# Kernel tuning notes

Measured on AMD Instinct MI355X. Metric: run time of the kernel, lower is better.

Reference implementation:

```python
import jax, jax.numpy as jnp
import numpy as np

B, S, D = 4, 2048, 1024
E, H, TOP_K = 8, 4096, 2


def setup_inputs() -> dict:
    key = jax.random.key(0)
    ks = jax.random.split(key, 5)
    scale = 0.02
    return {
        "x": jax.random.normal(ks[0], (B, S, D), dtype=jnp.float32),
        "Wr": jax.random.normal(ks[1], (D, E), dtype=jnp.float32) * scale,
        "br": jnp.zeros((E,), dtype=jnp.float32),
        "W1": jax.random.normal(ks[2], (E, D, H), dtype=jnp.float32) * scale,
        "b1": jnp.zeros((E, H), dtype=jnp.float32),
        "W2": jax.random.normal(ks[3], (E, H, D), dtype=jnp.float32) * scale,
        "b2": jnp.zeros((E, D), dtype=jnp.float32),
    }


def reference(x, Wr, br, W1, b1, W2, b2):
    b, s, d = x.shape
    xf = x.reshape(-1, d)                                   # [T, D]
    gate = jax.nn.softmax(xf @ Wr + br, axis=-1)            # [T, E]
    top_w, top_i = jax.lax.top_k(gate, TOP_K)               # [T, K]
    top_w = top_w / jnp.sum(top_w, axis=-1, keepdims=True)
    # combine[t, e] = sum_i top_w[t, i] * 1{top_i[t, i] == e}
    combine = jnp.sum(jax.nn.one_hot(top_i, E, dtype=xf.dtype) * top_w[..., None], axis=1)  # [T, E]
    # Dense all-expert FFN (same math as the masked per-expert loops in torch)
    h = jax.nn.gelu(jnp.einsum('td,edh->teh', xf, W1) + b1, approximate=False)  # [T, E, H]
    out = jnp.einsum('teh,ehd,te->td', h, W2, combine) + combine @ b2           # [T, D]
    return out.reshape(b, s, d)
```

## Files before the change

### kernel.cpp

```cpp
#include <hip/hip_runtime.h>
#include <cstdio>


#define T_TOK 8192
#define DIM   1024
#define NEXP  8
#define HID   4096
#define MAXR  18432

typedef float          f32x4   __attribute__((ext_vector_type(4)));
typedef short          bf16x8  __attribute__((ext_vector_type(8)));
typedef unsigned short u16x4   __attribute__((ext_vector_type(4)));

static __device__ __forceinline__ unsigned short f2bf(float f) {
  unsigned int u = __builtin_bit_cast(unsigned int, f);
  u = (u + 0x7FFFu + ((u >> 16) & 1u)) >> 16;
  return (unsigned short)u;
}

static __device__ __forceinline__ void gl16(const void* g, void* l) {
  __builtin_amdgcn_global_load_lds(
      (const __attribute__((address_space(1))) unsigned int*)g,
      (__attribute__((address_space(3))) unsigned int*)l,
      16, 0, 0);
}

#define FENCE() asm volatile("" ::: "memory")

__global__ __launch_bounds__(256) void router_k(const float* __restrict__ x,
                                                const float* __restrict__ Wr,
                                                const float* __restrict__ br,
                                                int* __restrict__ meta,
                                                int2* __restrict__ top_i,
                                                float2* __restrict__ top_w) {
  int lane = threadIdx.x & 63;
  int wid  = threadIdx.x >> 6;
  int t = blockIdx.x * 4 + wid;
  const float* xp = x + (size_t)t * DIM + lane * 16;
  float acc[NEXP];
#pragma unroll
  for (int e = 0; e < NEXP; ++e) acc[e] = 0.f;
#pragma unroll
  for (int j = 0; j < 16; j += 4) {
    float4 xv = *(const float4*)(xp + j);
    const float* wp = Wr + (size_t)(lane * 16 + j) * NEXP;
#pragma unroll
    for (int jj = 0; jj < 4; ++jj) {
      float xs = jj == 0 ? xv.x : jj == 1 ? xv.y : jj == 2 ? xv.z : xv.w;
      float4 w0 = *(const float4*)(wp + jj * NEXP);
      float4 w1 = *(const float4*)(wp + jj * NEXP + 4);
      acc[0] += xs * w0.x; acc[1] += xs * w0.y; acc[2] += xs * w0.z; acc[3] += xs * w0.w;
      acc[4] += xs * w1.x; acc[5] += xs * w1.y; acc[6] += xs * w1.z; acc[7] += xs * w1.w;
    }
  }
#pragma unroll
  for (int off = 32; off > 0; off >>= 1) {
#pragma unroll
    for (int e = 0; e < NEXP; ++e) acc[e] += __shfl_xor(acc[e], off);
  }
  if (lane == 0) {
    float l[NEXP];
#pragma unroll
    for (int e = 0; e < NEXP; ++e) l[e] = acc[e] + br[e];
    int e1 = 0;
#pragma unroll
    for (int e = 1; e < NEXP; ++e) if (l[e] > l[e1]) e1 = e;
    int e2 = (e1 == 0) ? 1 : 0;
#pragma unroll
    for (int e = 0; e < NEXP; ++e) if (e != e1 && l[e] > l[e2]) e2 = e;
    float g  = expf(l[e2] - l[e1]);
    float w1 = 1.f / (1.f + g);
    top_i[t] = make_int2(e1, e2);
    top_w[t] = make_float2(w1, 1.f - w1);
    atomicAdd(&meta[e1], 1);
    atomicAdd(&meta[e2], 1);
  }
}

__global__ void prefix_k(int* __restrict__ meta) {
  if (threadIdx.x == 0) {
    int s = 0;
#pragma unroll
    for (int e = 0; e < NEXP; ++e) {
      meta[16 + e] = s;
      s += (meta[e] + 255) & ~255;
    }
    meta[24] = s;
    meta[25] = s;
  }
}

__global__ __launch_bounds__(256) void fill_k(int* __restrict__ tok_of_row,
                                              float* __restrict__ wt_of_row) {
  int i = blockIdx.x * 256 + threadIdx.x;
  if (i < MAXR) { tok_of_row[i] = 0; wt_of_row[i] = 0.f; }
}

__global__ __launch_bounds__(256) void scatter_k(const int2* __restrict__ top_i,
                                                 const float2* __restrict__ top_w,
                                                 int* __restrict__ meta,
                                                 int* __restrict__ row_of,
                                                 int* __restrict__ tok_of_row,
                                                 float* __restrict__ wt_of_row) {
  int t = blockIdx.x * 256 + threadIdx.x;
  int2  ei = top_i[t];
  float2 w = top_w[t];
  int p = atomicAdd(&meta[8 + ei.x], 1);
  int r = meta[16 + ei.x] + p;
  tok_of_row[r] = t; wt_of_row[r] = w.x; row_of[t * 2] = r;
  p = atomicAdd(&meta[8 + ei.y], 1);
  r = meta[16 + ei.y] + p;
  tok_of_row[r] = t; wt_of_row[r] = w.y; row_of[t * 2 + 1] = r;
}

__global__ __launch_bounds__(256) void gather_k(const float* __restrict__ x,
                                                const int* __restrict__ tok_of_row,
                                                const int* __restrict__ meta,
                                                unsigned short* __restrict__ xg) {
  int r = blockIdx.x;
  if (r >= meta[25]) return;
  int t = tok_of_row[r];
  int c = threadIdx.x * 4;
  float4 v = *(const float4*)(x + (size_t)t * DIM + c);
  u16x4 o;
  o[0] = f2bf(v.x); o[1] = f2bf(v.y); o[2] = f2bf(v.z); o[3] = f2bf(v.w);
  *(u16x4*)(xg + (size_t)r * DIM + c) = o;
}

__global__ __launch_bounds__(256) void transpose_convert_k(const float* __restrict__ W,
                                                           unsigned short* __restrict__ WT,
                                                           int R, int C) {
  __shared__ float tile[32][33];
  int e = blockIdx.z;
  int c0 = blockIdx.x * 32, r0 = blockIdx.y * 32;
  const float* Wp = W + (size_t)e * R * C;
  unsigned short* Op = WT + (size_t)e * R * C;
  int tr = threadIdx.x >> 3;
  int tc = (threadIdx.x & 7) * 4;
  float4 v = *(const float4*)(Wp + (size_t)(r0 + tr) * C + c0 + tc);
  tile[tr][tc] = v.x; tile[tr][tc + 1] = v.y; tile[tr][tc + 2] = v.z; tile[tr][tc + 3] = v.w;
  __syncthreads();
  int oc  = threadIdx.x >> 3;
  int orr = (threadIdx.x & 7) * 4;
  u16x4 o;
#pragma unroll
  for (int j = 0; j < 4; ++j) o[j] = f2bf(tile[orr + j][oc]);
  *(u16x4*)(Op + (size_t)(c0 + oc) * R + r0 + orr) = o;
}


template <int KH, int MH>
__device__ __forceinline__ void do_phase(const unsigned short* lds_, int buf,
                                         int aoff, int boff, f32x4 (&acc)[8][4]) {
  const unsigned short* Ar = lds_ + (buf * 4 + KH) * 8192 + aoff + MH * 2048;
  const unsigned short* Br = lds_ + (buf * 4 + 2 + KH) * 8192 + boff;
  bf16x8 af[4], bv[4];
#pragma unroll
  for (int r = 0; r < 4; ++r) af[r] = *(const bf16x8*)(Ar + r * 512);
#pragma unroll
  for (int n = 0; n < 4; ++n) bv[n] = *(const bf16x8*)(Br + n * 512);
  __builtin_amdgcn_s_setprio(1);
#pragma unroll
  for (int r = 0; r < 4; ++r)
#pragma unroll
    for (int n = 0; n < 4; ++n)
      acc[MH * 4 + r][n] =
          __builtin_amdgcn_mfma_f32_16x16x32_bf16(af[r], bv[n], acc[MH * 4 + r][n], 0, 0, 0);
  __builtin_amdgcn_s_setprio(0);
}

template <int KTOT, int NTOT, int EPI>
__global__ __launch_bounds__(512, 2) void gemm8_k(const unsigned short* __restrict__ A,
                                                  const unsigned short* __restrict__ Bt,
                                                  const float* __restrict__ bias,
                                                  const int* __restrict__ meta,
                                                  const float* __restrict__ wt_of_row,
                                                  const int* __restrict__ tok_of_row,
                                                  void* __restrict__ Cout) {
  constexpr int NTILES = NTOT / 256;
  constexpr int NWG = (MAXR / 256) * NTILES;
  constexpr int NT = KTOT / 64;
  __shared__ __align__(16) unsigned short lds[65536];

  int id = ((int)blockIdx.x & 7) * (NWG / 8) + ((int)blockIdx.x >> 3);
  int row0 = (id / NTILES) * 256;
  int n0   = (id % NTILES) * 256;
  if (row0 >= meta[25]) return;
  int e = 0;
  while (meta[17 + e] <= row0) ++e;
  const unsigned short* Bp = Bt + (size_t)e * NTOT * KTOT;

  int tid = threadIdx.x;
  int lane = tid & 63, wid = tid >> 6;
  int wm = wid >> 2, wn = wid & 3;

  int r0s = tid >> 2, r1s = 128 + (tid >> 2);
  int s0 = (tid & 3) ^ ((r0s >> 1) & 3);
  int s1 = (tid & 3) ^ ((r1s >> 1) & 3);
  const unsigned short* pA0 = A + (size_t)(row0 + r0s) * KTOT + s0 * 8;
  const unsigned short* pA1 = A + (size_t)(row0 + r1s) * KTOT + s1 * 8;
  const unsigned short* pB0 = Bp + (size_t)(n0 + r0s) * KTOT + s0 * 8;
  const unsigned short* pB1 = Bp + (size_t)(n0 + r1s) * KTOT + s1 * 8;
  int ldst = wid * 512;

  auto stage = [&](int bufx, int mat, int kh, int kt) {
    int rb = (bufx * 4 + mat * 2 + kh) * 8192 + ldst;
    int ko = kt * 64 + kh * 32;
    gl16((mat ? pB0 : pA0) + ko, (void*)(lds + rb));
    gl16((mat ? pB1 : pA1) + ko, (void*)(lds + rb + 4096));
  };

  int sF = ((lane >> 4) ^ ((lane >> 1) & 3)) * 8;
  int aoff = wm * 4096 + (lane & 15) * 32 + sF;
  int boff = wn * 2048 + (lane & 15) * 32 + sF;

  f32x4 acc[8][4];
#pragma unroll
  for (int r = 0; r < 8; ++r)
#pragma unroll
    for (int n = 0; n < 4; ++n) acc[r][n] = (f32x4){0.f, 0.f, 0.f, 0.f};

  stage(0, 1, 0, 0); stage(0, 0, 0, 0); stage(0, 1, 1, 0); stage(0, 0, 1, 0);
  FENCE();

  for (int t = 0; t < NT - 1; ++t) {
    int buf = t & 1, nb = buf ^ 1;
    stage(nb, 1, 0, t + 1);
    asm volatile("s_waitcnt vmcnt(6)" ::: "memory");
    __builtin_amdgcn_s_barrier(); FENCE();
    do_phase<0, 0>(lds, buf, aoff, boff, acc);
    stage(nb, 0, 0, t + 1); FENCE();
    __builtin_amdgcn_s_barrier(); FENCE();
    do_phase<0, 1>(lds, buf, aoff, boff, acc);
    stage(nb, 1, 1, t + 1);
    asm volatile("s_waitcnt vmcnt(6)" ::: "memory");
    __builtin_amdgcn_s_barrier(); FENCE();
    do_phase<1, 0>(lds, buf, aoff, boff, acc);
    stage(nb, 0, 1, t + 1); FENCE();
    __builtin_amdgcn_s_barrier(); FENCE();
    do_phase<1, 1>(lds, buf, aoff, boff, acc);
  }
  {
    int buf = (NT - 1) & 1;
    asm volatile("s_waitcnt vmcnt(4)" ::: "memory");
    __builtin_amdgcn_s_barrier(); FENCE();
    do_phase<0, 0>(lds, buf, aoff, boff, acc);
    __builtin_amdgcn_s_barrier(); FENCE();
    do_phase<0, 1>(lds, buf, aoff, boff, acc);
    asm volatile("s_waitcnt vmcnt(0)" ::: "memory");
    __builtin_amdgcn_s_barrier(); FENCE();
    do_phase<1, 0>(lds, buf, aoff, boff, acc);
    __builtin_amdgcn_s_barrier(); FENCE();
    do_phase<1, 1>(lds, buf, aoff, boff, acc);
  }

  int rb2 = row0 + wm * 128 + ((lane >> 4) << 2);
  int nb2 = n0 + wn * 64 + (lane & 15);
  if constexpr (EPI == 0) {
    unsigned short* Hp = (unsigned short*)Cout;
    const float* bp = bias + (size_t)e * NTOT;
#pragma unroll
    for (int r = 0; r < 8; ++r)
#pragma unroll
      for (int n = 0; n < 4; ++n) {
        int ncol = nb2 + n * 16;
        float bv = bp[ncol];
#pragma unroll
        for (int g = 0; g < 4; ++g) {
          int m = rb2 + r * 16 + g;
          float v = acc[r][n][g] + bv;
          v = 0.5f * v * (1.f + erff(v * 0.70710678118654752f));
          Hp[(size_t)m * NTOT + ncol] = f2bf(v);
        }
      }
  } else {
    float* Op = (float*)Cout;
    const float* bp = bias + (size_t)e * NTOT;
#pragma unroll
    for (int r = 0; r < 8; ++r)
#pragma unroll
      for (int g = 0; g < 4; ++g) {
        int m = rb2 + r * 16 + g;
        float wt = wt_of_row[m];
        if (wt != 0.f) {
          float* orow = Op + (size_t)tok_of_row[m] * DIM;
#pragma unroll
          for (int n = 0; n < 4; ++n) {
            int ncol = nb2 + n * 16;
            atomicAdd(orow + ncol, (acc[r][n][g] + bp[ncol]) * wt);
          }
        }
      }
  }
}

extern "C" void kernel_launch(void* const* d_in, const int* in_sizes, int n_in,
                              void* d_out, int out_size, void* d_ws, size_t ws_size,
                              hipStream_t stream) {
  const float* x  = (const float*)d_in[0];
  const float* Wr = (const float*)d_in[1];
  const float* br = (const float*)d_in[2];
  const float* W1 = (const float*)d_in[3];
  const float* b1 = (const float*)d_in[4];
  const float* W2 = (const float*)d_in[5];
  const float* b2 = (const float*)d_in[6];
  float* out = (float*)d_out;

  char* base = (char*)d_ws;
  size_t off = 0;
  auto carve = [&](size_t bytes) -> void* {
    void* r = base + off;
    off = (off + bytes + 255) & ~(size_t)255;
    return r;
  };
  int*            meta       = (int*)carve(26 * 4);
  int2*           top_i      = (int2*)carve((size_t)T_TOK * 8);
  float2*         top_w      = (float2*)carve((size_t)T_TOK * 8);
  int*            row_of     = (int*)carve((size_t)T_TOK * 2 * 4);
  int*            tok_of_row = (int*)carve((size_t)MAXR * 4);
  float*          wt_of_row  = (float*)carve((size_t)MAXR * 4);
  unsigned short* xg         = (unsigned short*)carve((size_t)MAXR * DIM * 2);
  unsigned short* W1bT       = (unsigned short*)carve((size_t)NEXP * DIM * HID * 2);
  unsigned short* W2bT       = (unsigned short*)carve((size_t)NEXP * DIM * HID * 2);
  unsigned short* hbuf       = (unsigned short*)carve((size_t)MAXR * HID * 2);
  if (off > ws_size) {
    fprintf(stderr, "kernel_launch: ws_size too small: need %zu have %zu\n", off, ws_size);
    return;
  }

  hipMemsetAsync(meta, 0, 26 * 4, stream);
  hipMemsetAsync(out, 0, (size_t)out_size * 4, stream);
  hipLaunchKernelGGL(transpose_convert_k, dim3(HID / 32, DIM / 32, NEXP), dim3(256), 0, stream,
                     W1, W1bT, DIM, HID);
  hipLaunchKernelGGL(transpose_convert_k, dim3(DIM / 32, HID / 32, NEXP), dim3(256), 0, stream,
                     W2, W2bT, HID, DIM);
  hipLaunchKernelGGL(fill_k, dim3((MAXR + 255) / 256), dim3(256), 0, stream,
                     tok_of_row, wt_of_row);
  hipLaunchKernelGGL(router_k, dim3(T_TOK / 4), dim3(256), 0, stream,
                     x, Wr, br, meta, top_i, top_w);
  hipLaunchKernelGGL(prefix_k, dim3(1), dim3(64), 0, stream, meta);
  hipLaunchKernelGGL(scatter_k, dim3(T_TOK / 256), dim3(256), 0, stream,
                     top_i, top_w, meta, row_of, tok_of_row, wt_of_row);
  hipLaunchKernelGGL(gather_k, dim3(MAXR), dim3(256), 0, stream, x, tok_of_row, meta, xg);
  hipLaunchKernelGGL((gemm8_k<DIM, HID, 0>), dim3((MAXR / 256) * (HID / 256)), dim3(512), 0,
                     stream, xg, W1bT, b1, meta, wt_of_row, tok_of_row, (void*)hbuf);
  hipLaunchKernelGGL((gemm8_k<HID, DIM, 1>), dim3((MAXR / 256) * (DIM / 256)), dim3(512), 0,
                     stream, hbuf, W2bT, b2, meta, wt_of_row, tok_of_row, (void*)out);
}
```

Measured before the change: 952.5 us.

## Restructure GEMM main loop into ping-pong LDS pipeline with reg-prefetch and B reuse

Rewrites the bf16 MFMA GEMM inner loop as a templated per-k-tile routine. Each routine issues its LDS fragment reads before the barrier, waits on lgkmcnt, then runs the MFMA block. B fragments are now loaded once per k-half and reused across both M halves instead of reloaded, cutting LDS reads. The loop is unrolled by two with compile-time buffer indices and reworked vmcnt waits, adding more barriers per tile and new correctness risk in the wait counts and the odd/even tail handling.

```diff
diff --git a/kernel.cpp b/kernel.cpp
--- a/kernel.cpp
+++ b/kernel.cpp
@@ -26,6 +26,10 @@
 }
 
 #define FENCE() asm volatile("" ::: "memory")
+#define BAR()   do { FENCE(); __builtin_amdgcn_s_barrier(); FENCE(); } while (0)
+#define LGKM0() asm volatile("s_waitcnt lgkmcnt(0)" ::: "memory")
+#define VMW4()  asm volatile("s_waitcnt vmcnt(4)" ::: "memory")
+#define VMW0()  asm volatile("s_waitcnt vmcnt(0)" ::: "memory")
 
 __global__ __launch_bounds__(256) void router_k(const float* __restrict__ x,
                                                 const float* __restrict__ Wr,
@@ -149,24 +153,69 @@
 }
 
 
-template <int KH, int MH>
-__device__ __forceinline__ void do_phase(const unsigned short* lds_, int buf,
-                                         int aoff, int boff, f32x4 (&acc)[8][4]) {
-  const unsigned short* Ar = lds_ + (buf * 4 + KH) * 8192 + aoff + MH * 2048;
-  const unsigned short* Br = lds_ + (buf * 4 + 2 + KH) * 8192 + boff;
+template <int RB>
+__device__ __forceinline__ void mfma16(const bf16x8 (&af)[4], const bf16x8 (&bv)[4],
+                                       f32x4 (&acc)[8][4]) {
+  __builtin_amdgcn_s_setprio(1);
+#pragma unroll
+  for (int r = 0; r < 4; ++r)
+#pragma unroll
+    for (int n = 0; n < 4; ++n)
+      acc[RB + r][n] =
+          __builtin_amdgcn_mfma_f32_16x16x32_bf16(af[r], bv[n], acc[RB + r][n], 0, 0, 0);
+  __builtin_amdgcn_s_setprio(0);
+}
+
+template <int BUF, bool STAGE, bool LAST>
+__device__ __forceinline__ void tile_k(unsigned short* lds, int ko,
+                                       const unsigned short* pA0, const unsigned short* pA1,
+                                       const unsigned short* pB0, const unsigned short* pB1,
+                                       int ldst, int aoff, int boff, f32x4 (&acc)[8][4]) {
+  constexpr int NB = BUF ^ 1;
   bf16x8 af[4], bv[4];
-#pragma unroll
-  for (int r = 0; r < 4; ++r) af[r] = *(const bf16x8*)(Ar + r * 512);
-#pragma unroll
-  for (int n = 0; n < 4; ++n) bv[n] = *(const bf16x8*)(Br + n * 512);
-  __builtin_amdgcn_s_setprio(1);
+
+  auto stg = [&](int mat, int kh) {
+    if constexpr (STAGE) {
+      int rb = (NB * 4 + mat * 2 + kh) * 8192 + ldst;
+      const unsigned short* s0 = (mat ? pB0 : pA0) + ko + kh * 32;
+      const unsigned short* s1 = (mat ? pB1 : pA1) + ko + kh * 32;
+      gl16(s0, (void*)(lds + rb));
+      gl16(s1, (void*)(lds + rb + 4096));
+    }
+  };
+
+#pragma unroll
+  for (int n = 0; n < 4; ++n) bv[n] = *(const bf16x8*)(lds + (BUF * 4 + 2) * 8192 + boff + n * 512);
+#pragma unroll
+  for (int r = 0; r < 4; ++r) af[r] = *(const bf16x8*)(lds + (BUF * 4 + 0) * 8192 + aoff + r * 512);
+  stg(1, 0);
+  BAR(); LGKM0();
+  mfma16<0>(af, bv, acc);
+  BAR();
 #pragma unroll
   for (int r = 0; r < 4; ++r)
-#pragma unroll
-    for (int n = 0; n < 4; ++n)
-      acc[MH * 4 + r][n] =
-          __builtin_amdgcn_mfma_f32_16x16x32_bf16(af[r], bv[n], acc[MH * 4 + r][n], 0, 0, 0);
-  __builtin_amdgcn_s_setprio(0);
+    af[r] = *(const bf16x8*)(lds + (BUF * 4 + 0) * 8192 + aoff + 2048 + r * 512);
+  stg(0, 0);
+  BAR(); LGKM0();
+  mfma16<4>(af, bv, acc);
+  if constexpr (STAGE) { VMW4(); } else if constexpr (LAST) { VMW0(); }
+  BAR();
+#pragma unroll
+  for (int n = 0; n < 4; ++n) bv[n] = *(const bf16x8*)(lds + (BUF * 4 + 3) * 8192 + boff + n * 512);
+#pragma unroll
+  for (int r = 0; r < 4; ++r) af[r] = *(const bf16x8*)(lds + (BUF * 4 + 1) * 8192 + aoff + r * 512);
+  stg(1, 1);
+  BAR(); LGKM0();
+  mfma16<0>(af, bv, acc);
+  BAR();
+#pragma unroll
+  for (int r = 0; r < 4; ++r)
+    af[r] = *(const bf16x8*)(lds + (BUF * 4 + 1) * 8192 + aoff + 2048 + r * 512);
+  stg(0, 1);
+  BAR(); LGKM0();
+  mfma16<4>(af, bv, acc);
+  if constexpr (STAGE) VMW4();
+  BAR();
 }
 
 template <int KTOT, int NTOT, int EPI>
@@ -203,13 +252,6 @@
   const unsigned short* pB1 = Bp + (size_t)(n0 + r1s) * KTOT + s1 * 8;
   int ldst = wid * 512;
 
-  auto stage = [&](int bufx, int mat, int kh, int kt) {
-    int rb = (bufx * 4 + mat * 2 + kh) * 8192 + ldst;
-    int ko = kt * 64 + kh * 32;
-    gl16((mat ? pB0 : pA0) + ko, (void*)(lds + rb));
-    gl16((mat ? pB1 : pA1) + ko, (void*)(lds + rb + 4096));
-  };
-
   int sF = ((lane >> 4) ^ ((lane >> 1) & 3)) * 8;
   int aoff = wm * 4096 + (lane & 15) * 32 + sF;
   int boff = wn * 2048 + (lane & 15) * 32 + sF;
@@ -220,39 +262,18 @@
 #pragma unroll
     for (int n = 0; n < 4; ++n) acc[r][n] = (f32x4){0.f, 0.f, 0.f, 0.f};
 
-  stage(0, 1, 0, 0); stage(0, 0, 0, 0); stage(0, 1, 1, 0); stage(0, 0, 1, 0);
-  FENCE();
-
-  for (int t = 0; t < NT - 1; ++t) {
-    int buf = t & 1, nb = buf ^ 1;
-    stage(nb, 1, 0, t + 1);
-    asm volatile("s_waitcnt vmcnt(6)" ::: "memory");
-    __builtin_amdgcn_s_barrier(); FENCE();
-    do_phase<0, 0>(lds, buf, aoff, boff, acc);
-    stage(nb, 0, 0, t + 1); FENCE();
-    __builtin_amdgcn_s_barrier(); FENCE();
-    do_phase<0, 1>(lds, buf, aoff, boff, acc);
-    stage(nb, 1, 1, t + 1);
-    asm volatile("s_waitcnt vmcnt(6)" ::: "memory");
-    __builtin_amdgcn_s_barrier(); FENCE();
-    do_phase<1, 0>(lds, buf, aoff, boff, acc);
-    stage(nb, 0, 1, t + 1); FENCE();
-    __builtin_amdgcn_s_barrier(); FENCE();
-    do_phase<1, 1>(lds, buf, aoff, boff, acc);
-  }
-  {
-    int buf = (NT - 1) & 1;
-    asm volatile("s_waitcnt vmcnt(4)" ::: "memory");
-    __builtin_amdgcn_s_barrier(); FENCE();
-    do_phase<0, 0>(lds, buf, aoff, boff, acc);
-    __builtin_amdgcn_s_barrier(); FENCE();
-    do_phase<0, 1>(lds, buf, aoff, boff, acc);
-    asm volatile("s_waitcnt vmcnt(0)" ::: "memory");
-    __builtin_amdgcn_s_barrier(); FENCE();
-    do_phase<1, 0>(lds, buf, aoff, boff, acc);
-    __builtin_amdgcn_s_barrier(); FENCE();
-    do_phase<1, 1>(lds, buf, aoff, boff, acc);
-  }
+  gl16(pB0, (void*)(lds + 2 * 8192 + ldst)); gl16(pB1, (void*)(lds + 2 * 8192 + ldst + 4096));
+  gl16(pA0, (void*)(lds + 0 * 8192 + ldst)); gl16(pA1, (void*)(lds + 0 * 8192 + ldst + 4096));
+  gl16(pB0 + 32, (void*)(lds + 3 * 8192 + ldst)); gl16(pB1 + 32, (void*)(lds + 3 * 8192 + ldst + 4096));
+  gl16(pA0 + 32, (void*)(lds + 1 * 8192 + ldst)); gl16(pA1 + 32, (void*)(lds + 1 * 8192 + ldst + 4096));
+  VMW4(); BAR();
+
+  for (int t = 0; t < NT - 2; t += 2) {
+    tile_k<0, true, false>(lds, (t + 1) * 64, pA0, pA1, pB0, pB1, ldst, aoff, boff, acc);
+    tile_k<1, true, false>(lds, (t + 2) * 64, pA0, pA1, pB0, pB1, ldst, aoff, boff, acc);
+  }
+  tile_k<0, true, false>(lds, (NT - 1) * 64, pA0, pA1, pB0, pB1, ldst, aoff, boff, acc);
+  tile_k<1, false, true>(lds, 0, pA0, pA1, pB0, pB1, ldst, aoff, boff, acc);
 
   int rb2 = row0 + wm * 128 + ((lane >> 4) << 2);
   int nb2 = n0 + wn * 64 + (lane & 15);
```

After: 949.4 us. Within noise of the previous version (-0.3%).

## Rework GEMM main loop into two-barrier double-buffered pipeline and fuse prep kernels

Applied to the files above, without the earlier changes.

Replaces the eight-phase GEMM k-loop, which used four barriers per 64-wide k tile, with a double-buffered scheme. Each full tile of A and B is staged with global_load_lds into the other buffer while two k-steps run from the current one, using inline-asm ds_read_b128 with a new XOR swizzle and one barrier per tile. It also merges the weight transpose/convert, router and fill kernels into one prep kernel to cut launch overhead. The trade-off is coarser synchronization that waits on vmcnt(0) at every tile, so load latency may be exposed where the old scheme overlapped it more finely.

```diff
diff --git a/kernel.cpp b/kernel.cpp
--- a/kernel.cpp
+++ b/kernel.cpp
@@ -25,17 +25,42 @@
       16, 0, 0);
 }
 
-#define FENCE() asm volatile("" ::: "memory")
-
-__global__ __launch_bounds__(256) void router_k(const float* __restrict__ x,
-                                                const float* __restrict__ Wr,
-                                                const float* __restrict__ br,
-                                                int* __restrict__ meta,
-                                                int2* __restrict__ top_i,
-                                                float2* __restrict__ top_w) {
+template <int OFF>
+static __device__ __forceinline__ bf16x8 dsr128(unsigned addr) {
+  bf16x8 r;
+  asm volatile("ds_read_b128 %0, %1 offset:%2" : "=v"(r) : "v"(addr), "i"(OFF));
+  return r;
+}
+
+static __device__ __forceinline__ void transpose_body(const float* __restrict__ W,
+                                                      unsigned short* __restrict__ WT,
+                                                      int R, int C, int bx, int by, int e,
+                                                      float (*tile)[33]) {
+  int c0 = bx * 32, r0 = by * 32;
+  const float* Wp = W + (size_t)e * R * C;
+  unsigned short* Op = WT + (size_t)e * R * C;
+  int tr = threadIdx.x >> 3;
+  int tc = (threadIdx.x & 7) * 4;
+  float4 v = *(const float4*)(Wp + (size_t)(r0 + tr) * C + c0 + tc);
+  tile[tr][tc] = v.x; tile[tr][tc + 1] = v.y; tile[tr][tc + 2] = v.z; tile[tr][tc + 3] = v.w;
+  __syncthreads();
+  int oc  = threadIdx.x >> 3;
+  int orr = (threadIdx.x & 7) * 4;
+  u16x4 o;
+#pragma unroll
+  for (int j = 0; j < 4; ++j) o[j] = f2bf(tile[orr + j][oc]);
+  *(u16x4*)(Op + (size_t)(c0 + oc) * R + r0 + orr) = o;
+}
+
+static __device__ __forceinline__ void router_body(int blk, const float* __restrict__ x,
+                                                   const float* __restrict__ Wr,
+                                                   const float* __restrict__ br,
+                                                   int* __restrict__ meta,
+                                                   int2* __restrict__ top_i,
+                                                   float2* __restrict__ top_w) {
   int lane = threadIdx.x & 63;
   int wid  = threadIdx.x >> 6;
-  int t = blockIdx.x * 4 + wid;
+  int t = blk * 4 + wid;
   const float* xp = x + (size_t)t * DIM + lane * 16;
   float acc[NEXP];
 #pragma unroll
@@ -77,6 +102,33 @@
   }
 }
 
+__global__ __launch_bounds__(256) void prep_k(const float* __restrict__ W1,
+                                              const float* __restrict__ W2,
+                                              unsigned short* __restrict__ W1bT,
+                                              unsigned short* __restrict__ W2bT,
+                                              const float* __restrict__ x,
+                                              const float* __restrict__ Wr,
+                                              const float* __restrict__ br,
+                                              int* __restrict__ meta,
+                                              int2* __restrict__ top_i,
+                                              float2* __restrict__ top_w,
+                                              int* __restrict__ tok_of_row,
+                                              float* __restrict__ wt_of_row) {
+  __shared__ float tile[32][33];
+  int id = blockIdx.x;
+  if (id < 32768) {
+    transpose_body(W1, W1bT, DIM, HID, id & 127, (id >> 7) & 31, id >> 12, tile);
+  } else if (id < 65536) {
+    int id2 = id - 32768;
+    transpose_body(W2, W2bT, HID, DIM, id2 & 31, (id2 >> 5) & 127, id2 >> 12, tile);
+  } else if (id < 67584) {
+    router_body(id - 65536, x, Wr, br, meta, top_i, top_w);
+  } else {
+    int i = (id - 67584) * 256 + threadIdx.x;
+    if (i < MAXR) { tok_of_row[i] = 0; wt_of_row[i] = 0.f; }
+  }
+}
+
 __global__ void prefix_k(int* __restrict__ meta) {
   if (threadIdx.x == 0) {
     int s = 0;
@@ -88,12 +140,6 @@
     meta[24] = s;
     meta[25] = s;
   }
-}
-
-__global__ __launch_bounds__(256) void fill_k(int* __restrict__ tok_of_row,
-                                              float* __restrict__ wt_of_row) {
-  int i = blockIdx.x * 256 + threadIdx.x;
-  if (i < MAXR) { tok_of_row[i] = 0; wt_of_row[i] = 0.f; }
 }
 
 __global__ __launch_bounds__(256) void scatter_k(const int2* __restrict__ top_i,
@@ -127,56 +173,68 @@
   *(u16x4*)(xg + (size_t)r * DIM + c) = o;
 }
 
-__global__ __launch_bounds__(256) void transpose_convert_k(const float* __restrict__ W,
-                                                           unsigned short* __restrict__ WT,
-                                                           int R, int C) {
-  __shared__ float tile[32][33];
-  int e = blockIdx.z;
-  int c0 = blockIdx.x * 32, r0 = blockIdx.y * 32;
-  const float* Wp = W + (size_t)e * R * C;
-  unsigned short* Op = WT + (size_t)e * R * C;
-  int tr = threadIdx.x >> 3;
-  int tc = (threadIdx.x & 7) * 4;
-  float4 v = *(const float4*)(Wp + (size_t)(r0 + tr) * C + c0 + tc);
-  tile[tr][tc] = v.x; tile[tr][tc + 1] = v.y; tile[tr][tc + 2] = v.z; tile[tr][tc + 3] = v.w;
-  __syncthreads();
-  int oc  = threadIdx.x >> 3;
-  int orr = (threadIdx.x & 7) * 4;
-  u16x4 o;
-#pragma unroll
-  for (int j = 0; j < 4; ++j) o[j] = f2bf(tile[orr + j][oc]);
-  *(u16x4*)(Op + (size_t)(c0 + oc) * R + r0 + orr) = o;
-}
-
-
-template <int KH, int MH>
-__device__ __forceinline__ void do_phase(const unsigned short* lds_, int buf,
-                                         int aoff, int boff, f32x4 (&acc)[8][4]) {
-  const unsigned short* Ar = lds_ + (buf * 4 + KH) * 8192 + aoff + MH * 2048;
-  const unsigned short* Br = lds_ + (buf * 4 + 2 + KH) * 8192 + boff;
-  bf16x8 af[4], bv[4];
-#pragma unroll
-  for (int r = 0; r < 4; ++r) af[r] = *(const bf16x8*)(Ar + r * 512);
-#pragma unroll
-  for (int n = 0; n < 4; ++n) bv[n] = *(const bf16x8*)(Br + n * 512);
+
+template <int NB, int KTOT>
+static __device__ __forceinline__ void stage_tile(unsigned short* lds,
+                                                  const unsigned short* pA,
+                                                  const unsigned short* pB,
+                                                  int wid, int kt) {
+#pragma unroll
+  for (int h = 0; h < 2; ++h)
+#pragma unroll
+    for (int sw = 0; sw < 2; ++sw) {
+      int go = (h * 128 + sw * 64) * KTOT + kt * 64;
+      int lo = NB * 16384 + h * 8192 + sw * 4096 + wid * 512;
+      gl16(pA + go, lds + lo);
+      gl16(pB + go, lds + 32768 + lo);
+    }
+}
+
+template <int RB>
+static __device__ __forceinline__ void kstep(unsigned aA, unsigned aB, f32x4 (&acc)[8][4]) {
+  bf16x8 a[8], b[4];
+  a[0] = dsr128<RB +     0>(aA); a[1] = dsr128<RB +  2048>(aA);
+  a[2] = dsr128<RB +  4096>(aA); a[3] = dsr128<RB +  6144>(aA);
+  a[4] = dsr128<RB +  8192>(aA); a[5] = dsr128<RB + 10240>(aA);
+  a[6] = dsr128<RB + 12288>(aA); a[7] = dsr128<RB + 14336>(aA);
+  b[0] = dsr128<RB +     0>(aB); b[1] = dsr128<RB +  2048>(aB);
+  b[2] = dsr128<RB +  4096>(aB); b[3] = dsr128<RB +  6144>(aB);
+  asm volatile("s_waitcnt lgkmcnt(0)" ::);
+  __builtin_amdgcn_sched_barrier(0);
   __builtin_amdgcn_s_setprio(1);
 #pragma unroll
-  for (int r = 0; r < 4; ++r)
-#pragma unroll
-    for (int n = 0; n < 4; ++n)
-      acc[MH * 4 + r][n] =
-          __builtin_amdgcn_mfma_f32_16x16x32_bf16(af[r], bv[n], acc[MH * 4 + r][n], 0, 0, 0);
+  for (int fr = 0; fr < 8; ++fr)
+#pragma unroll
+    for (int j = 0; j < 4; ++j)
+      acc[fr][j] = __builtin_amdgcn_mfma_f32_16x16x32_bf16(a[fr], b[j], acc[fr][j], 0, 0, 0);
   __builtin_amdgcn_s_setprio(0);
 }
 
+template <int B, bool STG, int KTOT>
+static __device__ __forceinline__ void gtile(unsigned short* lds,
+                                             const unsigned short* pA,
+                                             const unsigned short* pB,
+                                             int wid, int kt_next,
+                                             unsigned aA0, unsigned aA1,
+                                             unsigned aB0, unsigned aB1,
+                                             f32x4 (&acc)[8][4]) {
+  if constexpr (STG) stage_tile<B ^ 1, KTOT>(lds, pA, pB, wid, kt_next);
+  kstep<B * 32768>(aA0, aB0, acc);
+  kstep<B * 32768>(aA1, aB1, acc);
+  if constexpr (STG) {
+    asm volatile("s_waitcnt vmcnt(0)" ::);
+    __builtin_amdgcn_s_barrier();
+  }
+}
+
 template <int KTOT, int NTOT, int EPI>
-__global__ __launch_bounds__(512, 2) void gemm8_k(const unsigned short* __restrict__ A,
-                                                  const unsigned short* __restrict__ Bt,
-                                                  const float* __restrict__ bias,
-                                                  const int* __restrict__ meta,
-                                                  const float* __restrict__ wt_of_row,
-                                                  const int* __restrict__ tok_of_row,
-                                                  void* __restrict__ Cout) {
+__global__ __launch_bounds__(512, 2) void gemm2p_k(const unsigned short* __restrict__ A,
+                                                   const unsigned short* __restrict__ Bt,
+                                                   const float* __restrict__ bias,
+                                                   const int* __restrict__ meta,
+                                                   const float* __restrict__ wt_of_row,
+                                                   const int* __restrict__ tok_of_row,
+                                                   void* __restrict__ Cout) {
   constexpr int NTILES = NTOT / 256;
   constexpr int NWG = (MAXR / 256) * NTILES;
   constexpr int NT = KTOT / 64;
@@ -194,25 +252,19 @@
   int lane = tid & 63, wid = tid >> 6;
   int wm = wid >> 2, wn = wid & 3;
 
-  int r0s = tid >> 2, r1s = 128 + (tid >> 2);
-  int s0 = (tid & 3) ^ ((r0s >> 1) & 3);
-  int s1 = (tid & 3) ^ ((r1s >> 1) & 3);
-  const unsigned short* pA0 = A + (size_t)(row0 + r0s) * KTOT + s0 * 8;
-  const unsigned short* pA1 = A + (size_t)(row0 + r1s) * KTOT + s1 * 8;
-  const unsigned short* pB0 = Bp + (size_t)(n0 + r0s) * KTOT + s0 * 8;
-  const unsigned short* pB1 = Bp + (size_t)(n0 + r1s) * KTOT + s1 * 8;
-  int ldst = wid * 512;
-
-  auto stage = [&](int bufx, int mat, int kh, int kt) {
-    int rb = (bufx * 4 + mat * 2 + kh) * 8192 + ldst;
-    int ko = kt * 64 + kh * 32;
-    gl16((mat ? pB0 : pA0) + ko, (void*)(lds + rb));
-    gl16((mat ? pB1 : pA1) + ko, (void*)(lds + rb + 4096));
-  };
-
-  int sF = ((lane >> 4) ^ ((lane >> 1) & 3)) * 8;
-  int aoff = wm * 4096 + (lane & 15) * 32 + sF;
-  int boff = wn * 2048 + (lane & 15) * 32 + sF;
+  int colS = ((tid & 7) ^ ((tid >> 3) & 7)) * 8;
+  const unsigned short* pA = A  + (size_t)(row0 + (tid >> 3)) * KTOT + colS;
+  const unsigned short* pB = Bp + (size_t)(n0   + (tid >> 3)) * KTOT + colS;
+
+  int g = lane >> 4, am = lane & 15;
+  unsigned lb = (unsigned)(unsigned long long)
+      (__attribute__((address_space(3))) unsigned short*)lds;
+  unsigned sc0 = (unsigned)(((0 * 4 + g) ^ (am & 7)) * 16);
+  unsigned sc1 = (unsigned)(((1 * 4 + g) ^ (am & 7)) * 16);
+  unsigned aA0 = lb + (unsigned)((wm * 128 + am) * 128) + sc0;
+  unsigned aA1 = lb + (unsigned)((wm * 128 + am) * 128) + sc1;
+  unsigned aB0 = lb + 65536u + (unsigned)((wn * 64 + am) * 128) + sc0;
+  unsigned aB1 = lb + 65536u + (unsigned)((wn * 64 + am) * 128) + sc1;
 
   f32x4 acc[8][4];
 #pragma unroll
@@ -220,42 +272,19 @@
 #pragma unroll
     for (int n = 0; n < 4; ++n) acc[r][n] = (f32x4){0.f, 0.f, 0.f, 0.f};
 
-  stage(0, 1, 0, 0); stage(0, 0, 0, 0); stage(0, 1, 1, 0); stage(0, 0, 1, 0);
-  FENCE();
-
-  for (int t = 0; t < NT - 1; ++t) {
-    int buf = t & 1, nb = buf ^ 1;
-    stage(nb, 1, 0, t + 1);
-    asm volatile("s_waitcnt vmcnt(6)" ::: "memory");
-    __builtin_amdgcn_s_barrier(); FENCE();
-    do_phase<0, 0>(lds, buf, aoff, boff, acc);
-    stage(nb, 0, 0, t + 1); FENCE();
-    __builtin_amdgcn_s_barrier(); FENCE();
-    do_phase<0, 1>(lds, buf, aoff, boff, acc);
-    stage(nb, 1, 1, t + 1);
-    asm volatile("s_waitcnt vmcnt(6)" ::: "memory");
-    __builtin_amdgcn_s_barrier(); FENCE();
-    do_phase<1, 0>(lds, buf, aoff, boff, acc);
-    stage(nb, 0, 1, t + 1); FENCE();
-    __builtin_amdgcn_s_barrier(); FENCE();
-    do_phase<1, 1>(lds, buf, aoff, boff, acc);
-  }
-  {
-    int buf = (NT - 1) & 1;
-    asm volatile("s_waitcnt vmcnt(4)" ::: "memory");
-    __builtin_amdgcn_s_barrier(); FENCE();
-    do_phase<0, 0>(lds, buf, aoff, boff, acc);
-    __builtin_amdgcn_s_barrier(); FENCE();
-    do_phase<0, 1>(lds, buf, aoff, boff, acc);
-    asm volatile("s_waitcnt vmcnt(0)" ::: "memory");
-    __builtin_amdgcn_s_barrier(); FENCE();
-    do_phase<1, 0>(lds, buf, aoff, boff, acc);
-    __builtin_amdgcn_s_barrier(); FENCE();
-    do_phase<1, 1>(lds, buf, aoff, boff, acc);
-  }
+  stage_tile<0, KTOT>(lds, pA, pB, wid, 0);
+  asm volatile("s_waitcnt vmcnt(0)" ::);
+  __builtin_amdgcn_s_barrier();
+
+  for (int t = 0; t < NT - 2; t += 2) {
+    gtile<0, true, KTOT>(lds, pA, pB, wid, t + 1, aA0, aA1, aB0, aB1, acc);
+    gtile<1, true, KTOT>(lds, pA, pB, wid, t + 2, aA0, aA1, aB0, aB1, acc);
+  }
+  gtile<0, true, KTOT>(lds, pA, pB, wid, NT - 1, aA0, aA1, aB0, aB1, acc);
+  gtile<1, false, KTOT>(lds, pA, pB, wid, 0, aA0, aA1, aB0, aB1, acc);
 
   int rb2 = row0 + wm * 128 + ((lane >> 4) << 2);
-  int nb2 = n0 + wn * 64 + (lane & 15);
+  int nb2 = n0 + wn * 64 + am;
   if constexpr (EPI == 0) {
     unsigned short* Hp = (unsigned short*)Cout;
     const float* bp = bias + (size_t)e * NTOT;
@@ -266,9 +295,9 @@
         int ncol = nb2 + n * 16;
         float bv = bp[ncol];
 #pragma unroll
-        for (int g = 0; g < 4; ++g) {
-          int m = rb2 + r * 16 + g;
-          float v = acc[r][n][g] + bv;
+        for (int gg = 0; gg < 4; ++gg) {
+          int m = rb2 + r * 16 + gg;
+          float v = acc[r][n][gg] + bv;
           v = 0.5f * v * (1.f + erff(v * 0.70710678118654752f));
           Hp[(size_t)m * NTOT + ncol] = f2bf(v);
         }
@@ -279,15 +308,15 @@
 #pragma unroll
     for (int r = 0; r < 8; ++r)
 #pragma unroll
-      for (int g = 0; g < 4; ++g) {
-        int m = rb2 + r * 16 + g;
+      for (int gg = 0; gg < 4; ++gg) {
+        int m = rb2 + r * 16 + gg;
         float wt = wt_of_row[m];
         if (wt != 0.f) {
           float* orow = Op + (size_t)tok_of_row[m] * DIM;
 #pragma unroll
           for (int n = 0; n < 4; ++n) {
             int ncol = nb2 + n * 16;
-            atomicAdd(orow + ncol, (acc[r][n][g] + bp[ncol]) * wt);
+            atomicAdd(orow + ncol, (acc[r][n][gg] + bp[ncol]) * wt);
           }
         }
       }
@@ -330,20 +359,15 @@
 
   hipMemsetAsync(meta, 0, 26 * 4, stream);
   hipMemsetAsync(out, 0, (size_t)out_size * 4, stream);
-  hipLaunchKernelGGL(transpose_convert_k, dim3(HID / 32, DIM / 32, NEXP), dim3(256), 0, stream,
-                     W1, W1bT, DIM, HID);
-  hipLaunchKernelGGL(transpose_convert_k, dim3(DIM / 32, HID / 32, NEXP), dim3(256), 0, stream,
-                     W2, W2bT, HID, DIM);
-  hipLaunchKernelGGL(fill_k, dim3((MAXR + 255) / 256), dim3(256), 0, stream,
+  hipLaunchKernelGGL(prep_k, dim3(67656), dim3(256), 0, stream,
+                     W1, W2, W1bT, W2bT, x, Wr, br, meta, top_i, top_w,
                      tok_of_row, wt_of_row);
-  hipLaunchKernelGGL(router_k, dim3(T_TOK / 4), dim3(256), 0, stream,
-                     x, Wr, br, meta, top_i, top_w);
   hipLaunchKernelGGL(prefix_k, dim3(1), dim3(64), 0, stream, meta);
   hipLaunchKernelGGL(scatter_k, dim3(T_TOK / 256), dim3(256), 0, stream,
                      top_i, top_w, meta, row_of, tok_of_row, wt_of_row);
   hipLaunchKernelGGL(gather_k, dim3(MAXR), dim3(256), 0, stream, x, tok_of_row, meta, xg);
-  hipLaunchKernelGGL((gemm8_k<DIM, HID, 0>), dim3((MAXR / 256) * (HID / 256)), dim3(512), 0,
+  hipLaunchKernelGGL((gemm2p_k<DIM, HID, 0>), dim3((MAXR / 256) * (HID / 256)), dim3(512), 0,
                      stream, xg, W1bT, b1, meta, wt_of_row, tok_of_row, (void*)hbuf);
-  hipLaunchKernelGGL((gemm8_k<HID, DIM, 1>), dim3((MAXR / 256) * (DIM / 256)), dim3(512), 0,
+  hipLaunchKernelGGL((gemm2p_k<HID, DIM, 1>), dim3((MAXR / 256) * (DIM / 256)), dim3(512), 0,
                      stream, hbuf, W2bT, b2, meta, wt_of_row, tok_of_row, (void*)out);
 }
```

New measurement: 931.2 us. -2.2%, faster.
